# Performance work log

Hardware: AMD Instinct MI355X
Metric: run time of the kernel (lower is better)

## Reference

```python
import jax, jax.numpy as jnp
import numpy as np

N = 50000          # total points (25 clouds x 2000 pts)
C = 64             # feature channels (in == out, no bottleneck)
K_NN = 16          # neighbors kept per dilation branch
DILATIONS = (1, 2, 4)
KMAX = K_NN * max(DILATIONS)   # base kNN graph has k*d_max neighbors per node
B = 25             # number of point clouds
EPS = 1e-16


def setup_inputs() -> dict:
    key = jax.random.key(0)
    ks = jax.random.split(key, 8)
    x = jax.random.normal(ks[0], (N, C), jnp.float32)
    pos = jax.random.normal(ks[1], (N, 3), jnp.float32)
    # kNN-style edge_index [2, N*KMAX]: row0 = source/neighbor j, row1 = center i,
    # KMAX consecutive edges per center node, neighbors restricted to the same cloud.
    pts = N // B
    cloud_base = (jnp.arange(N) // pts) * pts
    src = cloud_base[:, None] + jax.random.randint(ks[2], (N, KMAX), 0, pts)
    dst = jnp.broadcast_to(jnp.arange(N)[:, None], (N, KMAX))
    edge_index = jnp.stack([src.reshape(-1), dst.reshape(-1)]).astype(jnp.int32)
    batch = jnp.repeat(jnp.arange(B), pts).astype(jnp.int32)
    nD = len(DILATIONS)
    s = 1.0 / np.sqrt(C)
    Wv = jax.random.normal(ks[3], (nD, C, C), jnp.float32) * s   # lin (value)
    Wq = jax.random.normal(ks[4], (nD, C, C), jnp.float32) * s   # lin_dst
    Wk = jax.random.normal(ks[5], (nD, C, C), jnp.float32) * s   # lin_src
    Wp = jax.random.normal(ks[6], (nD, 3, C), jnp.float32) * (1.0 / np.sqrt(3.0))  # pos_nn
    bp = jax.random.normal(ks[7], (nD, C), jnp.float32) * 0.01
    return dict(x=x, pos=pos, Wv=Wv, Wq=Wq, Wk=Wk, Wp=Wp, bp=bp,
                edge_index=edge_index, batch=batch)


def _dilated_edges(edge_index, k, d):
    # take every d-th of the first k*d neighbors within each node's block -> k edges/node
    e = edge_index.reshape(2, -1, KMAX)[:, :, : k * d : d]
    return e.reshape(2, -1)


def _segment_softmax(a, seg, n):
    amax = jax.ops.segment_max(a, seg, num_segments=n)
    e = jnp.exp(a - amax[seg])
    s = jax.ops.segment_sum(e, seg, num_segments=n)
    return e / (s[seg] + EPS)


def _pt_conv(x, pos, src, dst, Wv, Wq, Wk, Wp, bp):
    # PyG PointTransformerConv: msg = softmax_i(q_i - k_j + delta_ij) * (v_j + delta_ij)
    n = x.shape[0]
    q = x @ Wq        # [N, C]  (lin_dst)
    kk = x @ Wk       # [N, C]  (lin_src)
    v = x @ Wv        # [N, C]  (lin, value)
    delta = (pos[dst] - pos[src]) @ Wp + bp            # [E, C] positional encoding
    alpha = _segment_softmax(q[dst] - kk[src] + delta, dst, n)
    return jax.ops.segment_sum(alpha * (v[src] + delta), dst, num_segments=n)


def reference(x, pos, Wv, Wq, Wk, Wp, bp, edge_index, batch):
    inputs = x
    res = None
    for i, d in enumerate(DILATIONS):
        e = _dilated_edges(edge_index, K_NN, d)
        h = _pt_conv(x, pos, e[0], e[1], Wv[i], Wq[i], Wk[i], Wp[i], bp[i])
        res = h if res is None else jnp.maximum(res, h)   # stack+max over branches
    # global max pool per cloud, gathered back per node
    pool = jax.ops.segment_max(x, batch, num_segments=B)[batch]
    res = jnp.maximum(res, pool)
    return res + inputs   # residual
```

## Files before the change

### kernel.cpp

```cpp
#include <hip/hip_runtime.h>
#include <math.h>

#define NP 50000
#define CH 64
#define KMAX 64
#define KNN 16
#define NB 25
#define PTS (NP / NB)
#define EPSF 1e-16f
#define NTILES (NP / 16)
#define TPW 4
#define L2E 1.4426950408889634f
#define LN2 0.6931471805599453f

typedef __attribute__((ext_vector_type(8))) short short8;
typedef __attribute__((ext_vector_type(4))) float float4v;
typedef __attribute__((ext_vector_type(4))) unsigned int uint4v;
typedef __attribute__((ext_vector_type(2))) unsigned int uint2v;
typedef __attribute__((ext_vector_type(4))) int int4v;
typedef __attribute__((ext_vector_type(4))) unsigned short ushort4v;

__device__ __forceinline__ ushort f2b(float f) {
  unsigned u = __float_as_uint(f);
  unsigned r = (u + 0x7FFFu + ((u >> 16) & 1u)) >> 16;
  return (ushort)r;
}
__device__ __forceinline__ float b2f(ushort h) {
  return __uint_as_float(((unsigned)h) << 16);
}

#define QBF_BYTES   ((size_t)3 * NP * CH * 2)
#define KVP_BYTES   ((size_t)3 * NP * CH * 4)
#define XBF_BYTES   ((size_t)NP * CH * 2)
#define WPACK_ELEMS (9 * 4 * 2 * 64 * 8)
#define XV (NP * CH / 4)

__global__ __launch_bounds__(256) void prep_kernel(
    const float* __restrict__ x,
    const float* __restrict__ Wv,
    const float* __restrict__ Wq,
    const float* __restrict__ Wk,
    ushort* __restrict__ x_bf,
    ushort* __restrict__ wpack,
    float* __restrict__ pool) {
  const int tid = threadIdx.x;
  const int bid = blockIdx.x;
  __shared__ float red[4][CH];

  if (bid < NB) {
    const int lane = tid & 63;
    const int wave = tid >> 6;
    const float* xb = x + (size_t)bid * PTS * CH;
    float m0 = -INFINITY, m1 = -INFINITY, m2 = -INFINITY, m3 = -INFINITY;
    for (int r = wave * 4; r < PTS; r += 16) {
      m0 = fmaxf(m0, xb[(size_t)(r + 0) * CH + lane]);
      m1 = fmaxf(m1, xb[(size_t)(r + 1) * CH + lane]);
      m2 = fmaxf(m2, xb[(size_t)(r + 2) * CH + lane]);
      m3 = fmaxf(m3, xb[(size_t)(r + 3) * CH + lane]);
    }
    red[wave][lane] = fmaxf(fmaxf(m0, m1), fmaxf(m2, m3));
    __syncthreads();
    if (wave == 0) {
      pool[bid * CH + lane] = fmaxf(fmaxf(red[0][lane], red[1][lane]),
                                    fmaxf(red[2][lane], red[3][lane]));
    }
  } else {
    const int gid = (bid - NB) * 256 + tid;
    if (gid < XV) {
      const float4* xv = (const float4*)x;
      float4 v = xv[gid];
      ushort4v o;
      o[0] = f2b(v.x); o[1] = f2b(v.y); o[2] = f2b(v.z); o[3] = f2b(v.w);
      *(ushort4v*)(x_bf + (size_t)gid * 4) = o;
    } else {
      int pid = gid - XV;
      if (pid < WPACK_ELEMS) {
        int j     = pid & 7;
        int lane  = (pid >> 3) & 63;
        int kstep = (pid >> 9) & 1;
        int mtile = (pid >> 10) & 3;
        int mat   = pid >> 12;
        const float* W;
        int d;
        float scale;
        if (mat < 3)      { W = Wq; d = mat;     scale = L2E; }
        else if (mat < 6) { W = Wk; d = mat - 3; scale = L2E; }
        else              { W = Wv; d = mat - 6; scale = 1.f; }
        int oc = mtile * 16 + (lane & 15);
        int ic = kstep * 32 + ((lane >> 4) & 3) * 8 + j;
        wpack[pid] = f2b(W[d * CH * CH + ic * CH + oc] * scale);
      }
    }
  }
}

__global__ __launch_bounds__(256) void qkv_mfma(
    const ushort* __restrict__ x_bf,
    const ushort* __restrict__ wpack,
    ushort* __restrict__ qbf,
    unsigned int* __restrict__ kvp) {
  const int lane = threadIdx.x;
  const int wave = threadIdx.y;
  const int y    = blockIdx.y;
  const int kbase = (lane >> 4) * 8;
  const int tile0 = (blockIdx.x * 4 + wave) * TPW;

  if (y < 3) {
    short8 af[4][2];
#pragma unroll
    for (int mt = 0; mt < 4; ++mt)
#pragma unroll
      for (int ks = 0; ks < 2; ++ks)
        af[mt][ks] = *(const short8*)(wpack +
            ((((size_t)y * 4 + mt) * 2 + ks) * 64 + lane) * 8);
    ushort* outM = qbf + (size_t)y * NP * CH;
#pragma unroll
    for (int t = 0; t < TPW; ++t) {
      int tile = tile0 + t;
      if (tile >= NTILES) break;
      int myNode = tile * 16 + (lane & 15);
      const ushort* xr = x_bf + (size_t)myNode * CH;
      short8 b0 = *(const short8*)(xr + kbase);
      short8 b1 = *(const short8*)(xr + 32 + kbase);
#pragma unroll
      for (int mt = 0; mt < 4; ++mt) {
        float4v acc = {0.f, 0.f, 0.f, 0.f};
        acc = __builtin_amdgcn_mfma_f32_16x16x32_bf16(af[mt][0], b0, acc, 0, 0, 0);
        acc = __builtin_amdgcn_mfma_f32_16x16x32_bf16(af[mt][1], b1, acc, 0, 0, 0);
        int oc = mt * 16 + (lane >> 4) * 4;
        uint2v o;
        o[0] = (unsigned)f2b(acc[0]) | ((unsigned)f2b(acc[1]) << 16);
        o[1] = (unsigned)f2b(acc[2]) | ((unsigned)f2b(acc[3]) << 16);
        *(uint2v*)(outM + (size_t)myNode * CH + oc) = o;
      }
    }
  } else {
    const int k  = y - 3;
    const int dd = k >> 1;
    const int h  = k & 1;
    short8 afK[2][2], afV[2][2];
#pragma unroll
    for (int m2 = 0; m2 < 2; ++m2)
#pragma unroll
      for (int ks = 0; ks < 2; ++ks) {
        int mt = 2 * h + m2;
        afK[m2][ks] = *(const short8*)(wpack +
            ((((size_t)(3 + dd) * 4 + mt) * 2 + ks) * 64 + lane) * 8);
        afV[m2][ks] = *(const short8*)(wpack +
            ((((size_t)(6 + dd) * 4 + mt) * 2 + ks) * 64 + lane) * 8);
      }
    unsigned int* outKV = kvp + (size_t)dd * NP * CH;
#pragma unroll
    for (int t = 0; t < TPW; ++t) {
      int tile = tile0 + t;
      if (tile >= NTILES) break;
      int myNode = tile * 16 + (lane & 15);
      const ushort* xr = x_bf + (size_t)myNode * CH;
      short8 b0 = *(const short8*)(xr + kbase);
      short8 b1 = *(const short8*)(xr + 32 + kbase);
#pragma unroll
      for (int m2 = 0; m2 < 2; ++m2) {
        float4v aK = {0.f, 0.f, 0.f, 0.f};
        float4v aV = {0.f, 0.f, 0.f, 0.f};
        aK = __builtin_amdgcn_mfma_f32_16x16x32_bf16(afK[m2][0], b0, aK, 0, 0, 0);
        aK = __builtin_amdgcn_mfma_f32_16x16x32_bf16(afK[m2][1], b1, aK, 0, 0, 0);
        aV = __builtin_amdgcn_mfma_f32_16x16x32_bf16(afV[m2][0], b0, aV, 0, 0, 0);
        aV = __builtin_amdgcn_mfma_f32_16x16x32_bf16(afV[m2][1], b1, aV, 0, 0, 0);
        int oc = (2 * h + m2) * 16 + (lane >> 4) * 4;
        uint4v o;
#pragma unroll
        for (int i = 0; i < 4; ++i)
          o[i] = ((unsigned)f2b(aK[i]) << 16) | (unsigned)f2b(aV[i]);
        *(uint4v*)(outKV + (size_t)myNode * CH + oc) = o;
      }
    }
  }
}

__global__ __launch_bounds__(256) void attn_kernel(
    const float* __restrict__ x,
    const float* __restrict__ pos,
    const float* __restrict__ Wp,
    const float* __restrict__ bp,
    const int*   __restrict__ edge_src,
    const ushort* __restrict__ qbf,
    const unsigned int* __restrict__ kvp,
    const float* __restrict__ pool,
    float* __restrict__ out) {
  const int tid = threadIdx.y * 64 + threadIdx.x;
  __shared__ float sEdge[16 * KMAX * 4];

  {
    const int nl = tid >> 4;
    const int p0 = (tid & 15) * 4;
    const int nd = blockIdx.x * 16 + nl;
    int4v jj = *(const int4v*)(edge_src + (size_t)nd * KMAX + p0);
    float px = pos[nd * 3 + 0];
    float py = pos[nd * 3 + 1];
    float pz = pos[nd * 3 + 2];
#pragma unroll
    for (int u = 0; u < 4; ++u) {
      int j = jj[u];
      float4v w;
      w[0] = px - pos[j * 3 + 0];
      w[1] = py - pos[j * 3 + 1];
      w[2] = pz - pos[j * 3 + 2];
      w[3] = __int_as_float(j << 8);
      *(float4v*)&sEdge[(nl * KMAX + p0 + u) * 4] = w;
    }
  }
  __syncthreads();

  const int lane = threadIdx.x;
  const int g  = lane >> 4;
  const int cl = lane & 15;
  const int nodeSlot = threadIdx.y * 4 + g;
  const int node = blockIdx.x * 16 + nodeSlot;
  const float* sMy = &sEdge[nodeSlot * KMAX * 4];
  const unsigned clOfs = (unsigned)(cl << 4);

  float4v res = {0.f, 0.f, 0.f, 0.f};

#pragma unroll
  for (int dd = 0; dd < 3; ++dd) {
    float4v q, wp0, wp1, wp2, bq;
    {
      ushort4v qh = *(const ushort4v*)(qbf + ((size_t)dd * NP + node) * CH + cl * 4);
#pragma unroll
      for (int i = 0; i < 4; ++i) q[i] = b2f(qh[i]);
      const float* WpD = Wp + dd * 192;
      wp0 = *(const float4v*)(WpD + 0 * 64 + cl * 4) * L2E;
      wp1 = *(const float4v*)(WpD + 1 * 64 + cl * 4) * L2E;
      wp2 = *(const float4v*)(WpD + 2 * 64 + cl * 4) * L2E;
      float4v bpv = *(const float4v*)(bp + dd * 64 + cl * 4);
      bq = q + bpv * L2E;
    }
    const char* KVb = (const char*)(kvp + (size_t)dd * NP * CH);
    const int dil = 1 << dd;

    float4v s    = {0.f, 0.f, 0.f, 0.f};
    float4v accv = {0.f, 0.f, 0.f, 0.f};
    float4v accd = {0.f, 0.f, 0.f, 0.f};
#pragma unroll
    for (int e = 0; e < KNN; ++e) {
      const int p = e * dil;
      float4v w = *(const float4v*)(sMy + p * 4);
      unsigned ofs = __float_as_uint(w[3]) + clOfs;
      uint4v u = *(const uint4v*)(KVb + ofs);
      float4v kf, vf, wgt;
#pragma unroll
      for (int i = 0; i < 4; ++i) kf[i] = __uint_as_float(u[i] & 0xFFFF0000u);
#pragma unroll
      for (int i = 0; i < 4; ++i) vf[i] = __uint_as_float(u[i] << 16);
      float4v t = bq + w[0] * wp0 + w[1] * wp1 + w[2] * wp2;
      float4v a = t - kf;
#pragma unroll
      for (int i = 0; i < 4; ++i) wgt[i] = __builtin_amdgcn_exp2f(a[i]);
      s    += wgt;
      accv += wgt * vf;
      float4v dlt = t - q;
      accd += wgt * dlt;
    }
    float4v r;
#pragma unroll
    for (int i = 0; i < 4; ++i)
      r[i] = (accv[i] + LN2 * accd[i]) * __builtin_amdgcn_rcpf(s[i] + EPSF);
    if (dd == 0) {
      res = r;
    } else {
#pragma unroll
      for (int i = 0; i < 4; ++i) res[i] = fmaxf(res[i], r[i]);
    }
  }

  const int b = node / PTS;
  float4v pv = *(const float4v*)(pool + b * CH + cl * 4);
  float4v xv = *(const float4v*)(x + (size_t)node * CH + cl * 4);
#pragma unroll
  for (int i = 0; i < 4; ++i) res[i] = fmaxf(res[i], pv[i]) + xv[i];
  *(float4v*)(out + (size_t)node * CH + cl * 4) = res;
}

extern "C" void kernel_launch(void* const* d_in, const int* in_sizes, int n_in,
                              void* d_out, int out_size, void* d_ws, size_t ws_size,
                              hipStream_t stream) {
  const float* x    = (const float*)d_in[0];
  const float* pos  = (const float*)d_in[1];
  const float* Wv   = (const float*)d_in[2];
  const float* Wq   = (const float*)d_in[3];
  const float* Wk   = (const float*)d_in[4];
  const float* Wp   = (const float*)d_in[5];
  const float* bp   = (const float*)d_in[6];
  const int*   ei   = (const int*)d_in[7];
  float* out = (float*)d_out;

  char* wsb = (char*)d_ws;
  ushort* qbf   = (ushort*)wsb;
  unsigned int* kvp = (unsigned int*)(wsb + QBF_BYTES);
  ushort* x_bf  = (ushort*)(wsb + QBF_BYTES + KVP_BYTES);
  ushort* wpack = (ushort*)(wsb + QBF_BYTES + KVP_BYTES + XBF_BYTES);
  float*  pool  = (float*)(wsb + QBF_BYTES + KVP_BYTES + XBF_BYTES +
                           (size_t)WPACK_ELEMS * 2);

  {
    int convBlocks = (XV + WPACK_ELEMS + 255) / 256;
    dim3 grid(NB + convBlocks);
    hipLaunchKernelGGL(prep_kernel, grid, dim3(256), 0, stream,
                       x, Wv, Wq, Wk, x_bf, wpack, pool);
  }
  {
    dim3 grid((NTILES + 4 * TPW - 1) / (4 * TPW), 9);
    dim3 block(64, 4);
    hipLaunchKernelGGL(qkv_mfma, grid, block, 0, stream, x_bf, wpack, qbf, kvp);
  }
  {
    dim3 grid(NP / 16);
    dim3 block(64, 4);
    hipLaunchKernelGGL(attn_kernel, grid, block, 0, stream,
                       x, pos, Wp, bp, ei, qbf, kvp, pool, out);
  }
}
```

Baseline: 225.9 us.

## Split dilation branches across waves and remap attention blocks per XCD

The attention kernel now gives each of three waves one dilation branch for the same 4 nodes, then combines the branch results through shared memory, rather than having one wave loop over all three branches for 16 nodes. Block indices are remapped so each XCD handles a contiguous range of nodes, which is meant to improve L2 locality of the gathered K/V rows. The QKV projection kernel is merged into one path per dilation that computes Q, K and V from a single x load, cutting the grid from 9 to 3 in y. The softmax delta accumulation is rewritten algebraically to accumulate w*t and subtract q*s at the end. The cost is smaller blocks, an extra barrier and more registers per QKV wave.

```diff
diff --git a/kernel.cpp b/kernel.cpp
--- a/kernel.cpp
+++ b/kernel.cpp
@@ -9,6 +9,7 @@
 #define PTS (NP / NB)
 #define EPSF 1e-16f
 #define NTILES (NP / 16)
+#define ATILES (NP / 4)
 #define TPW 4
 #define L2E 1.4426950408889634f
 #define LN2 0.6931471805599453f
@@ -17,7 +18,6 @@
 typedef __attribute__((ext_vector_type(4))) float float4v;
 typedef __attribute__((ext_vector_type(4))) unsigned int uint4v;
 typedef __attribute__((ext_vector_type(2))) unsigned int uint2v;
-typedef __attribute__((ext_vector_type(4))) int int4v;
 typedef __attribute__((ext_vector_type(4))) unsigned short ushort4v;
 
 __device__ __forceinline__ ushort f2b(float f) {
@@ -101,83 +101,64 @@
     unsigned int* __restrict__ kvp) {
   const int lane = threadIdx.x;
   const int wave = threadIdx.y;
-  const int y    = blockIdx.y;
+  const int dd   = blockIdx.y;
   const int kbase = (lane >> 4) * 8;
   const int tile0 = (blockIdx.x * 4 + wave) * TPW;
 
-  if (y < 3) {
-    short8 af[4][2];
-#pragma unroll
-    for (int mt = 0; mt < 4; ++mt)
-#pragma unroll
-      for (int ks = 0; ks < 2; ++ks)
-        af[mt][ks] = *(const short8*)(wpack +
-            ((((size_t)y * 4 + mt) * 2 + ks) * 64 + lane) * 8);
-    ushort* outM = qbf + (size_t)y * NP * CH;
-#pragma unroll
-    for (int t = 0; t < TPW; ++t) {
-      int tile = tile0 + t;
-      if (tile >= NTILES) break;
-      int myNode = tile * 16 + (lane & 15);
-      const ushort* xr = x_bf + (size_t)myNode * CH;
-      short8 b0 = *(const short8*)(xr + kbase);
-      short8 b1 = *(const short8*)(xr + 32 + kbase);
-#pragma unroll
-      for (int mt = 0; mt < 4; ++mt) {
-        float4v acc = {0.f, 0.f, 0.f, 0.f};
-        acc = __builtin_amdgcn_mfma_f32_16x16x32_bf16(af[mt][0], b0, acc, 0, 0, 0);
-        acc = __builtin_amdgcn_mfma_f32_16x16x32_bf16(af[mt][1], b1, acc, 0, 0, 0);
-        int oc = mt * 16 + (lane >> 4) * 4;
-        uint2v o;
-        o[0] = (unsigned)f2b(acc[0]) | ((unsigned)f2b(acc[1]) << 16);
-        o[1] = (unsigned)f2b(acc[2]) | ((unsigned)f2b(acc[3]) << 16);
-        *(uint2v*)(outM + (size_t)myNode * CH + oc) = o;
-      }
-    }
-  } else {
-    const int k  = y - 3;
-    const int dd = k >> 1;
-    const int h  = k & 1;
-    short8 afK[2][2], afV[2][2];
-#pragma unroll
-    for (int m2 = 0; m2 < 2; ++m2)
-#pragma unroll
-      for (int ks = 0; ks < 2; ++ks) {
-        int mt = 2 * h + m2;
-        afK[m2][ks] = *(const short8*)(wpack +
-            ((((size_t)(3 + dd) * 4 + mt) * 2 + ks) * 64 + lane) * 8);
-        afV[m2][ks] = *(const short8*)(wpack +
-            ((((size_t)(6 + dd) * 4 + mt) * 2 + ks) * 64 + lane) * 8);
-      }
-    unsigned int* outKV = kvp + (size_t)dd * NP * CH;
-#pragma unroll
-    for (int t = 0; t < TPW; ++t) {
-      int tile = tile0 + t;
-      if (tile >= NTILES) break;
-      int myNode = tile * 16 + (lane & 15);
-      const ushort* xr = x_bf + (size_t)myNode * CH;
-      short8 b0 = *(const short8*)(xr + kbase);
-      short8 b1 = *(const short8*)(xr + 32 + kbase);
-#pragma unroll
-      for (int m2 = 0; m2 < 2; ++m2) {
-        float4v aK = {0.f, 0.f, 0.f, 0.f};
-        float4v aV = {0.f, 0.f, 0.f, 0.f};
-        aK = __builtin_amdgcn_mfma_f32_16x16x32_bf16(afK[m2][0], b0, aK, 0, 0, 0);
-        aK = __builtin_amdgcn_mfma_f32_16x16x32_bf16(afK[m2][1], b1, aK, 0, 0, 0);
-        aV = __builtin_amdgcn_mfma_f32_16x16x32_bf16(afV[m2][0], b0, aV, 0, 0, 0);
-        aV = __builtin_amdgcn_mfma_f32_16x16x32_bf16(afV[m2][1], b1, aV, 0, 0, 0);
-        int oc = (2 * h + m2) * 16 + (lane >> 4) * 4;
-        uint4v o;
-#pragma unroll
-        for (int i = 0; i < 4; ++i)
-          o[i] = ((unsigned)f2b(aK[i]) << 16) | (unsigned)f2b(aV[i]);
-        *(uint4v*)(outKV + (size_t)myNode * CH + oc) = o;
-      }
-    }
-  }
-}
-
-__global__ __launch_bounds__(256) void attn_kernel(
+  short8 afQ[4][2], afK[4][2], afV[4][2];
+#pragma unroll
+  for (int mt = 0; mt < 4; ++mt)
+#pragma unroll
+    for (int ks = 0; ks < 2; ++ks) {
+      afQ[mt][ks] = *(const short8*)(wpack +
+          ((((size_t)dd * 4 + mt) * 2 + ks) * 64 + lane) * 8);
+      afK[mt][ks] = *(const short8*)(wpack +
+          ((((size_t)(3 + dd) * 4 + mt) * 2 + ks) * 64 + lane) * 8);
+      afV[mt][ks] = *(const short8*)(wpack +
+          ((((size_t)(6 + dd) * 4 + mt) * 2 + ks) * 64 + lane) * 8);
+    }
+
+  ushort* outQ = qbf + (size_t)dd * NP * CH;
+  unsigned int* outKV = kvp + (size_t)dd * NP * CH;
+
+#pragma unroll
+  for (int t = 0; t < TPW; ++t) {
+    int tile = tile0 + t;
+    if (tile >= NTILES) break;
+    int myNode = tile * 16 + (lane & 15);
+    const ushort* xr = x_bf + (size_t)myNode * CH;
+    short8 b0 = *(const short8*)(xr + kbase);
+    short8 b1 = *(const short8*)(xr + 32 + kbase);
+#pragma unroll
+    for (int mt = 0; mt < 4; ++mt) {
+      float4v aQ = {0.f, 0.f, 0.f, 0.f};
+      aQ = __builtin_amdgcn_mfma_f32_16x16x32_bf16(afQ[mt][0], b0, aQ, 0, 0, 0);
+      aQ = __builtin_amdgcn_mfma_f32_16x16x32_bf16(afQ[mt][1], b1, aQ, 0, 0, 0);
+      int oc = mt * 16 + (lane >> 4) * 4;
+      uint2v oq;
+      oq[0] = (unsigned)f2b(aQ[0]) | ((unsigned)f2b(aQ[1]) << 16);
+      oq[1] = (unsigned)f2b(aQ[2]) | ((unsigned)f2b(aQ[3]) << 16);
+      *(uint2v*)(outQ + (size_t)myNode * CH + oc) = oq;
+    }
+#pragma unroll
+    for (int mt = 0; mt < 4; ++mt) {
+      float4v aK = {0.f, 0.f, 0.f, 0.f};
+      float4v aV = {0.f, 0.f, 0.f, 0.f};
+      aK = __builtin_amdgcn_mfma_f32_16x16x32_bf16(afK[mt][0], b0, aK, 0, 0, 0);
+      aK = __builtin_amdgcn_mfma_f32_16x16x32_bf16(afK[mt][1], b1, aK, 0, 0, 0);
+      aV = __builtin_amdgcn_mfma_f32_16x16x32_bf16(afV[mt][0], b0, aV, 0, 0, 0);
+      aV = __builtin_amdgcn_mfma_f32_16x16x32_bf16(afV[mt][1], b1, aV, 0, 0, 0);
+      int oc = mt * 16 + (lane >> 4) * 4;
+      uint4v o;
+#pragma unroll
+      for (int i = 0; i < 4; ++i)
+        o[i] = ((unsigned)f2b(aK[i]) << 16) | (unsigned)f2b(aV[i]);
+      *(uint4v*)(outKV + (size_t)myNode * CH + oc) = o;
+    }
+  }
+}
+
+__global__ __launch_bounds__(192) void attn_kernel(
     const float* __restrict__ x,
     const float* __restrict__ pos,
     const float* __restrict__ Wp,
@@ -187,98 +168,96 @@
     const unsigned int* __restrict__ kvp,
     const float* __restrict__ pool,
     float* __restrict__ out) {
+  const int bx  = blockIdx.x;
+  const int xcd = bx & 7;
+  const int kk  = bx >> 3;
+  const int base = (ATILES * xcd) >> 3;
+  const int cnt  = ((ATILES * (xcd + 1)) >> 3) - base;
+  if (kk >= cnt) return;
+  const int node0 = (base + kk) * 4;
+
   const int tid = threadIdx.y * 64 + threadIdx.x;
-  __shared__ float sEdge[16 * KMAX * 4];
-
+  __shared__ float sEdge[4 * 260];
+  __shared__ float sRes[2 * 4 * 68];
+
+  for (int r = tid; r < 4 * KMAX; r += 192) {
+    int nl = r >> 6, p = r & 63;
+    int nd = node0 + nl;
+    int j = edge_src[(size_t)nd * KMAX + p];
+    float4v w;
+    w[0] = pos[nd * 3 + 0] - pos[j * 3 + 0];
+    w[1] = pos[nd * 3 + 1] - pos[j * 3 + 1];
+    w[2] = pos[nd * 3 + 2] - pos[j * 3 + 2];
+    w[3] = __int_as_float(j << 8);
+    *(float4v*)&sEdge[nl * 260 + p * 4] = w;
+  }
+  __syncthreads();
+
+  const int dd   = threadIdx.y;
+  const int lane = threadIdx.x;
+  const int g    = lane >> 4;
+  const int cl   = lane & 15;
+  const int node = node0 + g;
+  const float* sMy = &sEdge[g * 260];
+  const unsigned clOfs = (unsigned)(cl << 4);
+
+  float4v q, bq, wp0, wp1, wp2;
   {
-    const int nl = tid >> 4;
-    const int p0 = (tid & 15) * 4;
-    const int nd = blockIdx.x * 16 + nl;
-    int4v jj = *(const int4v*)(edge_src + (size_t)nd * KMAX + p0);
-    float px = pos[nd * 3 + 0];
-    float py = pos[nd * 3 + 1];
-    float pz = pos[nd * 3 + 2];
-#pragma unroll
-    for (int u = 0; u < 4; ++u) {
-      int j = jj[u];
-      float4v w;
-      w[0] = px - pos[j * 3 + 0];
-      w[1] = py - pos[j * 3 + 1];
-      w[2] = pz - pos[j * 3 + 2];
-      w[3] = __int_as_float(j << 8);
-      *(float4v*)&sEdge[(nl * KMAX + p0 + u) * 4] = w;
-    }
-  }
+    ushort4v qh = *(const ushort4v*)(qbf + ((size_t)dd * NP + node) * CH + cl * 4);
+#pragma unroll
+    for (int i = 0; i < 4; ++i) q[i] = b2f(qh[i]);
+    const float* WpD = Wp + dd * 192;
+    wp0 = *(const float4v*)(WpD + 0 * 64 + cl * 4) * L2E;
+    wp1 = *(const float4v*)(WpD + 1 * 64 + cl * 4) * L2E;
+    wp2 = *(const float4v*)(WpD + 2 * 64 + cl * 4) * L2E;
+    float4v bpv = *(const float4v*)(bp + dd * 64 + cl * 4);
+    bq = q + bpv * L2E;
+  }
+  const char* KVb = (const char*)(kvp + (size_t)dd * NP * CH);
+
+  float4v s    = {0.f, 0.f, 0.f, 0.f};
+  float4v accv = {0.f, 0.f, 0.f, 0.f};
+  float4v acct = {0.f, 0.f, 0.f, 0.f};
+#pragma unroll
+  for (int e = 0; e < KNN; ++e) {
+    const int p = e << dd;
+    float4v w = *(const float4v*)(sMy + p * 4);
+    uint4v u = *(const uint4v*)(KVb + (__float_as_uint(w[3]) + clOfs));
+    float4v kf, vf, wgt;
+#pragma unroll
+    for (int i = 0; i < 4; ++i) kf[i] = __uint_as_float(u[i] & 0xFFFF0000u);
+#pragma unroll
+    for (int i = 0; i < 4; ++i) vf[i] = __uint_as_float(u[i] << 16);
+    float4v t = bq + w[0] * wp0 + w[1] * wp1 + w[2] * wp2;
+    float4v a = t - kf;
+#pragma unroll
+    for (int i = 0; i < 4; ++i) wgt[i] = __builtin_amdgcn_exp2f(a[i]);
+    s    += wgt;
+    accv += wgt * vf;
+    acct += wgt * t;
+  }
+  float4v r;
+#pragma unroll
+  for (int i = 0; i < 4; ++i) {
+    float accd = acct[i] - q[i] * s[i];
+    r[i] = (accv[i] + LN2 * accd) * __builtin_amdgcn_rcpf(s[i] + EPSF);
+  }
+
+  if (dd > 0)
+    *(float4v*)&sRes[((dd - 1) * 4 + g) * 68 + cl * 4] = r;
   __syncthreads();
-
-  const int lane = threadIdx.x;
-  const int g  = lane >> 4;
-  const int cl = lane & 15;
-  const int nodeSlot = threadIdx.y * 4 + g;
-  const int node = blockIdx.x * 16 + nodeSlot;
-  const float* sMy = &sEdge[nodeSlot * KMAX * 4];
-  const unsigned clOfs = (unsigned)(cl << 4);
-
-  float4v res = {0.f, 0.f, 0.f, 0.f};
-
-#pragma unroll
-  for (int dd = 0; dd < 3; ++dd) {
-    float4v q, wp0, wp1, wp2, bq;
-    {
-      ushort4v qh = *(const ushort4v*)(qbf + ((size_t)dd * NP + node) * CH + cl * 4);
-#pragma unroll
-      for (int i = 0; i < 4; ++i) q[i] = b2f(qh[i]);
-      const float* WpD = Wp + dd * 192;
-      wp0 = *(const float4v*)(WpD + 0 * 64 + cl * 4) * L2E;
-      wp1 = *(const float4v*)(WpD + 1 * 64 + cl * 4) * L2E;
-      wp2 = *(const float4v*)(WpD + 2 * 64 + cl * 4) * L2E;
-      float4v bpv = *(const float4v*)(bp + dd * 64 + cl * 4);
-      bq = q + bpv * L2E;
-    }
-    const char* KVb = (const char*)(kvp + (size_t)dd * NP * CH);
-    const int dil = 1 << dd;
-
-    float4v s    = {0.f, 0.f, 0.f, 0.f};
-    float4v accv = {0.f, 0.f, 0.f, 0.f};
-    float4v accd = {0.f, 0.f, 0.f, 0.f};
-#pragma unroll
-    for (int e = 0; e < KNN; ++e) {
-      const int p = e * dil;
-      float4v w = *(const float4v*)(sMy + p * 4);
-      unsigned ofs = __float_as_uint(w[3]) + clOfs;
-      uint4v u = *(const uint4v*)(KVb + ofs);
-      float4v kf, vf, wgt;
-#pragma unroll
-      for (int i = 0; i < 4; ++i) kf[i] = __uint_as_float(u[i] & 0xFFFF0000u);
-#pragma unroll
-      for (int i = 0; i < 4; ++i) vf[i] = __uint_as_float(u[i] << 16);
-      float4v t = bq + w[0] * wp0 + w[1] * wp1 + w[2] * wp2;
-      float4v a = t - kf;
-#pragma unroll
-      for (int i = 0; i < 4; ++i) wgt[i] = __builtin_amdgcn_exp2f(a[i]);
-      s    += wgt;
-      accv += wgt * vf;
-      float4v dlt = t - q;
-      accd += wgt * dlt;
-    }
-    float4v r;
+  if (dd == 0) {
+    float4v r1 = *(const float4v*)&sRes[(0 * 4 + g) * 68 + cl * 4];
+    float4v r2 = *(const float4v*)&sRes[(1 * 4 + g) * 68 + cl * 4];
+    const int b = node / PTS;
+    float4v pv = *(const float4v*)(pool + b * CH + cl * 4);
+    float4v xv = *(const float4v*)(x + (size_t)node * CH + cl * 4);
+    float4v res;
 #pragma unroll
     for (int i = 0; i < 4; ++i)
-      r[i] = (accv[i] + LN2 * accd[i]) * __builtin_amdgcn_rcpf(s[i] + EPSF);
-    if (dd == 0) {
-      res = r;
-    } else {
-#pragma unroll
-      for (int i = 0; i < 4; ++i) res[i] = fmaxf(res[i], r[i]);
-    }
-  }
-
-  const int b = node / PTS;
-  float4v pv = *(const float4v*)(pool + b * CH + cl * 4);
-  float4v xv = *(const float4v*)(x + (size_t)node * CH + cl * 4);
-#pragma unroll
-  for (int i = 0; i < 4; ++i) res[i] = fmaxf(res[i], pv[i]) + xv[i];
-  *(float4v*)(out + (size_t)node * CH + cl * 4) = res;
+      res[i] = fmaxf(fmaxf(fmaxf(r[i], r1[i]), r2[i]), pv[i]) + xv[i];
+    *(float4v*)(out + (size_t)node * CH + cl * 4) = res;
+  }
 }
 
 extern "C" void kernel_launch(void* const* d_in, const int* in_sizes, int n_in,
@@ -309,13 +288,13 @@
                        x, Wv, Wq, Wk, x_bf, wpack, pool);
   }
   {
-    dim3 grid((NTILES + 4 * TPW - 1) / (4 * TPW), 9);
+    dim3 grid((NTILES + 4 * TPW - 1) / (4 * TPW), 3);
     dim3 block(64, 4);
     hipLaunchKernelGGL(qkv_mfma, grid, block, 0, stream, x_bf, wpack, qbf, kvp);
   }
   {
-    dim3 grid(NP / 16);
-    dim3 block(64, 4);
+    dim3 grid(8 * ((ATILES + 7) / 8));
+    dim3 block(64, 3);
     hipLaunchKernelGGL(attn_kernel, grid, block, 0, stream,
                        x, pos, Wp, bp, ei, qbf, kvp, pool, out);
   }
```

New measurement: 226.3 us. No clear change (+0.2%).
